# Performance work log

Hardware: AMD Instinct MI355X
Metric: run time of the kernel (lower is better)

The kernel has to match this reference:

```python
import jax, jax.numpy as jnp
import numpy as np

# Grid spacing (CartesianGrid3D.dx / .dy)
DX = 1000.0
DY = 1000.0
WENO_EPS = 1e-6  # classic Jiang-Shu smoothness regularizer

NZ, NY, NX = 32, 1024, 1024


def _weno5_recon(qm2, qm1, q0, qp1, qp2):
    """Classic WENO5 (Jiang-Shu) reconstruction of q at the i+1/2 face,
    left-biased (stencil centered on cell i)."""
    c1312 = 13.0 / 12.0
    b0 = c1312 * (qm2 - 2.0 * qm1 + q0) ** 2 + 0.25 * (qm2 - 4.0 * qm1 + 3.0 * q0) ** 2
    b1 = c1312 * (qm1 - 2.0 * q0 + qp1) ** 2 + 0.25 * (qm1 - qp1) ** 2
    b2 = c1312 * (q0 - 2.0 * qp1 + qp2) ** 2 + 0.25 * (3.0 * q0 - 4.0 * qp1 + qp2) ** 2
    a0 = 0.1 / (WENO_EPS + b0) ** 2
    a1 = 0.6 / (WENO_EPS + b1) ** 2
    a2 = 0.3 / (WENO_EPS + b2) ** 2
    p0 = (2.0 * qm2 - 7.0 * qm1 + 11.0 * q0) / 6.0
    p1 = (-qm1 + 5.0 * q0 + 2.0 * qp1) / 6.0
    p2 = (2.0 * q0 + 5.0 * qp1 - qp2) / 6.0
    return (a0 * p0 + a1 * p1 + a2 * p2) / (a0 + a1 + a2)


def _weno5_flux(q, vel, axis):
    """Upwinded WENO5 flux vel * q_face at face i+1/2 along `axis`.
    Edge-padded so the flux array has the same shape as q (faithful to
    recon.weno5_x / weno5_y producing full-shape flux arrays whose interior
    is consumed by the divergence)."""
    q = jnp.moveaxis(q, axis, -1)
    vel = jnp.moveaxis(vel, axis, -1)
    n = q.shape[-1]
    pad = [(0, 0)] * (q.ndim - 1) + [(2, 3)]
    qp = jnp.pad(q, pad, mode='edge')
    sl = lambda o: qp[..., o:o + n]
    qm2, qm1, q0, qp1, qp2, qp3 = sl(0), sl(1), sl(2), sl(3), sl(4), sl(5)
    q_left = _weno5_recon(qm2, qm1, q0, qp1, qp2)          # upwind for vel >= 0
    q_right = _weno5_recon(qp3, qp2, qp1, q0, qm1)         # mirrored, vel < 0
    f = vel * jnp.where(vel >= 0.0, q_left, q_right)
    return jnp.moveaxis(f, -1, axis)


def setup_inputs() -> dict:
    key = jax.random.key(0)
    kh, ku, kv = jax.random.split(key, 3)
    h = jax.random.normal(kh, (NZ, NY, NX), dtype=jnp.float32)
    u = jax.random.normal(ku, (NZ, NY, NX), dtype=jnp.float32)
    v = jax.random.normal(kv, (NZ, NY, NX), dtype=jnp.float32)
    return {"h": h, "u": u, "v": v}


def reference(h, u, v):
    # fe: flux through east face (x), fn: flux through north face (y)
    fe = _weno5_flux(h, u, axis=2)
    fn = _weno5_flux(h, v, axis=1)
    div = ((fe[1:-1, 2:-2, 2:-2] - fe[1:-1, 2:-2, 1:-3]) / DX
           + (fn[1:-1, 2:-2, 2:-2] - fn[1:-1, 1:-3, 2:-2]) / DY)
    out = jnp.zeros_like(h)
    out = out.at[1:-1, 2:-2, 2:-2].set(-div)
    return out
```

## Files before the change

### kernel.cpp

```cpp
#include <hip/hip_runtime.h>

#define NZ 32
#define NY 1024
#define NX 1024
#define TY 16

__device__ __forceinline__ float rcpf(float x) { return __builtin_amdgcn_rcpf(x); }

__device__ __forceinline__ float weno5(float qm2, float qm1, float q0, float qp1, float qp2) {
    const float c1312 = 13.0f / 12.0f;
    float t0 = qm2 - 2.0f * qm1 + q0;
    float u0 = qm2 - 4.0f * qm1 + 3.0f * q0;
    float b0 = c1312 * t0 * t0 + 0.25f * u0 * u0;
    float t1 = qm1 - 2.0f * q0 + qp1;
    float u1 = qm1 - qp1;
    float b1 = c1312 * t1 * t1 + 0.25f * u1 * u1;
    float t2 = q0 - 2.0f * qp1 + qp2;
    float u2 = 3.0f * q0 - 4.0f * qp1 + qp2;
    float b2 = c1312 * t2 * t2 + 0.25f * u2 * u2;
    float e0 = 1e-6f + b0;
    float e1 = 1e-6f + b1;
    float e2 = 1e-6f + b2;
    float s0 = e0 * e0, s1 = e1 * e1, s2 = e2 * e2;
    float a0 = 0.1f * (s1 * s2);
    float a1 = 0.6f * (s0 * s2);
    float a2 = 0.3f * (s0 * s1);
    const float c16 = 1.0f / 6.0f;
    float p0 = (2.0f * qm2 - 7.0f * qm1 + 11.0f * q0) * c16;
    float p1 = (-qm1 + 5.0f * q0 + 2.0f * qp1) * c16;
    float p2 = (2.0f * q0 + 5.0f * qp1 - qp2) * c16;
    return (a0 * p0 + a1 * p1 + a2 * p2) * rcpf(a0 + a1 + a2);
}

__device__ __forceinline__ float upwind_flux(float vel, float qm2, float qm1, float q0,
                                             float qp1, float qp2, float qp3) {
    bool up = vel >= 0.0f;
    float s0 = up ? qm2 : qp3;
    float s1 = up ? qm1 : qp2;
    float s2 = up ? q0  : qp1;
    float s3 = up ? qp1 : q0;
    float s4 = up ? qp2 : qm1;
    return vel * weno5(s0, s1, s2, s3, s4);
}

__global__ __launch_bounds__(256) void adv_kernel(const float* __restrict__ h,
                                                  const float* __restrict__ u,
                                                  const float* __restrict__ v,
                                                  float* __restrict__ out) {
    const int tid = threadIdx.x;
    const int x  = blockIdx.x * 256 + tid;
    const int z  = blockIdx.z;
    const int y0 = blockIdx.y * TY;
    const size_t zoff = (size_t)z * (NY * NX);
    const float* __restrict__ hz = h + zoff;
    const float* __restrict__ uz = u + zoff;
    const float* __restrict__ vz = v + zoff;
    float* __restrict__ oz = out + zoff;

    if (z == 0 || z == NZ - 1) {
#pragma unroll
        for (int t = 0; t < TY; ++t) oz[(y0 + t) * NX + x] = 0.0f;
        return;
    }

    int xc[7];
#pragma unroll
    for (int k = 0; k < 7; ++k) {
        int xx = x - 3 + k;
        xc[k] = xx < 0 ? 0 : (xx > NX - 1 ? NX - 1 : xx);
    }
    const int xm1 = (x > 0) ? x - 1 : 0;
    const bool xin = (x >= 2) && (x <= NX - 3);
    const bool lane0 = (tid & 63) == 0;

    float hy[7];
#pragma unroll
    for (int k = 0; k < 7; ++k) {
        int yy = y0 - 3 + k;
        yy = yy < 0 ? 0 : (yy > NY - 1 ? NY - 1 : yy);
        hy[k] = hz[yy * NX + x];
    }

    {
    }
    const int ym1 = (y0 > 0) ? y0 - 1 : 0;
    float fn_lo = upwind_flux(vz[ym1 * NX + x], hy[0], hy[1], hy[2], hy[3], hy[4], hy[5]);

#pragma unroll
    for (int t = 0; t < TY; ++t) {
        const int y = y0 + t;
        const int row = y * NX;

        float hx0 = hz[row + xc[0]];
        float hx1 = hz[row + xc[1]];
        float hx2 = hz[row + xc[2]];
        float hx3 = hy[3];
        float hx4 = hz[row + xc[4]];
        float hx5 = hz[row + xc[5]];
        float hx6 = hz[row + xc[6]];

        float fe_hi = upwind_flux(uz[row + x], hx1, hx2, hx3, hx4, hx5, hx6);
        float fe_lo = __shfl_up(fe_hi, 1);
        if (lane0) {
            fe_lo = upwind_flux(uz[row + xm1], hx0, hx1, hx2, hx3, hx4, hx5);
        }

        float fn_hi = upwind_flux(vz[row + x], hy[1], hy[2], hy[3], hy[4], hy[5], hy[6]);

        const float inv_d = 1.0f / 1000.0f;
        float val = -((fe_hi - fe_lo) + (fn_hi - fn_lo)) * inv_d;
        bool interior = xin && (y >= 2) && (y <= NY - 3);
        oz[row + x] = interior ? val : 0.0f;

        fn_lo = fn_hi;
#pragma unroll
        for (int k = 0; k < 6; ++k) hy[k] = hy[k + 1];
        int yn = y + 4;
        yn = yn > NY - 1 ? NY - 1 : yn;
        hy[6] = hz[yn * NX + x];
    }
}

extern "C" void kernel_launch(void* const* d_in, const int* in_sizes, int n_in,
                              void* d_out, int out_size, void* d_ws, size_t ws_size,
                              hipStream_t stream) {
    const float* h = (const float*)d_in[0];
    const float* u = (const float*)d_in[1];
    const float* v = (const float*)d_in[2];
    float* out = (float*)d_out;

    dim3 block(256, 1, 1);
    dim3 grid(NX / 256, NY / TY, NZ);
    adv_kernel<<<grid, block, 0, stream>>>(h, u, v, out);
}
```

Baseline: 440.5 us.

## Process two x-points per thread with float2 loads and halve row tile

Each thread now handles two adjacent x columns and uses float2 vectorized loads for h, u, v and the output. The x-stencil is shared between the pair, so each row needs fewer loads and the even point's lo flux comes from the odd flux computed in the same thread. TY drops from 16 to 8 to keep the number of blocks up now that each block covers 512 columns, and the WENO polynomial coefficients are pre-folded into constants. The cost is higher register pressure from two float2 y-windows and the duplicated flux computations, plus a separate boundary path that uses scalar clamped loads.

```diff
diff --git a/kernel.cpp b/kernel.cpp
--- a/kernel.cpp
+++ b/kernel.cpp
@@ -3,7 +3,7 @@
 #define NZ 32
 #define NY 1024
 #define NX 1024
-#define TY 16
+#define TY 8
 
 __device__ __forceinline__ float rcpf(float x) { return __builtin_amdgcn_rcpf(x); }
 
@@ -18,17 +18,14 @@
     float t2 = q0 - 2.0f * qp1 + qp2;
     float u2 = 3.0f * q0 - 4.0f * qp1 + qp2;
     float b2 = c1312 * t2 * t2 + 0.25f * u2 * u2;
-    float e0 = 1e-6f + b0;
-    float e1 = 1e-6f + b1;
-    float e2 = 1e-6f + b2;
+    float e0 = 1e-6f + b0, e1 = 1e-6f + b1, e2 = 1e-6f + b2;
     float s0 = e0 * e0, s1 = e1 * e1, s2 = e2 * e2;
     float a0 = 0.1f * (s1 * s2);
     float a1 = 0.6f * (s0 * s2);
     float a2 = 0.3f * (s0 * s1);
-    const float c16 = 1.0f / 6.0f;
-    float p0 = (2.0f * qm2 - 7.0f * qm1 + 11.0f * q0) * c16;
-    float p1 = (-qm1 + 5.0f * q0 + 2.0f * qp1) * c16;
-    float p2 = (2.0f * q0 + 5.0f * qp1 - qp2) * c16;
+    float p0 = (1.0f / 3.0f) * qm2 + (-7.0f / 6.0f) * qm1 + (11.0f / 6.0f) * q0;
+    float p1 = (-1.0f / 6.0f) * qm1 + (5.0f / 6.0f) * q0 + (1.0f / 3.0f) * qp1;
+    float p2 = (1.0f / 3.0f) * q0 + (5.0f / 6.0f) * qp1 + (-1.0f / 6.0f) * qp2;
     return (a0 * p0 + a1 * p1 + a2 * p2) * rcpf(a0 + a1 + a2);
 }
 
@@ -48,9 +45,10 @@
                                                   const float* __restrict__ v,
                                                   float* __restrict__ out) {
     const int tid = threadIdx.x;
-    const int x  = blockIdx.x * 256 + tid;
-    const int z  = blockIdx.z;
-    const int y0 = blockIdx.y * TY;
+    const int px  = blockIdx.x * 256 + tid;
+    const int x0  = px * 2;
+    const int z   = blockIdx.z;
+    const int y0  = blockIdx.y * TY;
     const size_t zoff = (size_t)z * (NY * NX);
     const float* __restrict__ hz = h + zoff;
     const float* __restrict__ uz = u + zoff;
@@ -59,65 +57,88 @@
 
     if (z == 0 || z == NZ - 1) {
 #pragma unroll
-        for (int t = 0; t < TY; ++t) oz[(y0 + t) * NX + x] = 0.0f;
+        for (int t = 0; t < TY; ++t)
+            *(float2*)(oz + (y0 + t) * NX + x0) = make_float2(0.0f, 0.0f);
         return;
     }
 
-    int xc[7];
-#pragma unroll
-    for (int k = 0; k < 7; ++k) {
-        int xx = x - 3 + k;
-        xc[k] = xx < 0 ? 0 : (xx > NX - 1 ? NX - 1 : xx);
-    }
-    const int xm1 = (x > 0) ? x - 1 : 0;
-    const bool xin = (x >= 2) && (x <= NX - 3);
+    const bool xfast = (x0 >= 4) && (x0 <= NX - 6);
+    const bool xint  = (px >= 1) && (px <= (NX - 4) / 2);
     const bool lane0 = (tid & 63) == 0;
 
-    float hy[7];
+    float2 hy[7];
 #pragma unroll
     for (int k = 0; k < 7; ++k) {
         int yy = y0 - 3 + k;
         yy = yy < 0 ? 0 : (yy > NY - 1 ? NY - 1 : yy);
-        hy[k] = hz[yy * NX + x];
+        hy[k] = *(const float2*)(hz + yy * NX + x0);
     }
 
-    {
-    }
     const int ym1 = (y0 > 0) ? y0 - 1 : 0;
-    float fn_lo = upwind_flux(vz[ym1 * NX + x], hy[0], hy[1], hy[2], hy[3], hy[4], hy[5]);
+    float2 vm = *(const float2*)(vz + ym1 * NX + x0);
+    float fn_lo_e = upwind_flux(vm.x, hy[0].x, hy[1].x, hy[2].x, hy[3].x, hy[4].x, hy[5].x);
+    float fn_lo_o = upwind_flux(vm.y, hy[0].y, hy[1].y, hy[2].y, hy[3].y, hy[4].y, hy[5].y);
 
 #pragma unroll
     for (int t = 0; t < TY; ++t) {
-        const int y = y0 + t;
+        const int y   = y0 + t;
         const int row = y * NX;
+        const float* __restrict__ rp  = hz + row;
+        const float* __restrict__ rpu = uz + row;
 
-        float hx0 = hz[row + xc[0]];
-        float hx1 = hz[row + xc[1]];
-        float hx2 = hz[row + xc[2]];
-        float hx3 = hy[3];
-        float hx4 = hz[row + xc[4]];
-        float hx5 = hz[row + xc[5]];
-        float hx6 = hz[row + xc[6]];
+        float sl[10];
+        if (xfast) {
+            float2 m2  = *(const float2*)(rp + x0 - 4);
+            float2 m1  = *(const float2*)(rp + x0 - 2);
+            float2 pp1 = *(const float2*)(rp + x0 + 2);
+            float2 pp2 = *(const float2*)(rp + x0 + 4);
+            sl[0] = m2.x;  sl[1] = m2.y;
+            sl[2] = m1.x;  sl[3] = m1.y;
+            sl[6] = pp1.x; sl[7] = pp1.y;
+            sl[8] = pp2.x; sl[9] = pp2.y;
+        } else {
+#pragma unroll
+            for (int k = 0; k < 10; ++k) {
+                if (k == 4 || k == 5) continue;
+                int xx = x0 - 4 + k;
+                xx = xx < 0 ? 0 : (xx > NX - 1 ? NX - 1 : xx);
+                sl[k] = rp[xx];
+            }
+        }
+        sl[4] = hy[3].x;
+        sl[5] = hy[3].y;
 
-        float fe_hi = upwind_flux(uz[row + x], hx1, hx2, hx3, hx4, hx5, hx6);
-        float fe_lo = __shfl_up(fe_hi, 1);
+        float2 uv = *(const float2*)(rpu + x0);
+        float2 vv = *(const float2*)(vz + row + x0);
+
+        float f_e = upwind_flux(uv.x, sl[2], sl[3], sl[4], sl[5], sl[6], sl[7]);
+        float f_o = upwind_flux(uv.y, sl[3], sl[4], sl[5], sl[6], sl[7], sl[8]);
+
+        float fe_lo = __shfl_up(f_o, 1);
         if (lane0) {
-            fe_lo = upwind_flux(uz[row + xm1], hx0, hx1, hx2, hx3, hx4, hx5);
+            int xm = x0 - 1;
+            xm = xm < 0 ? 0 : xm;
+            fe_lo = upwind_flux(rpu[xm], sl[1], sl[2], sl[3], sl[4], sl[5], sl[6]);
         }
 
-        float fn_hi = upwind_flux(vz[row + x], hy[1], hy[2], hy[3], hy[4], hy[5], hy[6]);
+        float fn_e = upwind_flux(vv.x, hy[1].x, hy[2].x, hy[3].x, hy[4].x, hy[5].x, hy[6].x);
+        float fn_o = upwind_flux(vv.y, hy[1].y, hy[2].y, hy[3].y, hy[4].y, hy[5].y, hy[6].y);
 
         const float inv_d = 1.0f / 1000.0f;
-        float val = -((fe_hi - fe_lo) + (fn_hi - fn_lo)) * inv_d;
-        bool interior = xin && (y >= 2) && (y <= NY - 3);
-        oz[row + x] = interior ? val : 0.0f;
+        bool yin = (y >= 2) && (y <= NY - 3);
+        bool wr  = xint && yin;
+        float2 res;
+        res.x = wr ? -((f_e - fe_lo) + (fn_e - fn_lo_e)) * inv_d : 0.0f;
+        res.y = wr ? -((f_o - f_e) + (fn_o - fn_lo_o)) * inv_d : 0.0f;
+        *(float2*)(oz + row + x0) = res;
 
-        fn_lo = fn_hi;
+        fn_lo_e = fn_e;
+        fn_lo_o = fn_o;
 #pragma unroll
         for (int k = 0; k < 6; ++k) hy[k] = hy[k + 1];
         int yn = y + 4;
         yn = yn > NY - 1 ? NY - 1 : yn;
-        hy[6] = hz[yn * NX + x];
+        hy[6] = *(const float2*)(hz + yn * NX + x0);
     }
 }
 
@@ -130,6 +151,6 @@
     float* out = (float*)d_out;
 
     dim3 block(256, 1, 1);
-    dim3 grid(NX / 256, NY / TY, NZ);
+    dim3 grid(NX / 512, NY / TY, NZ);
     adv_kernel<<<grid, block, 0, stream>>>(h, u, v, out);
 }
```

Result: faster. 396.6 us (-10.0%).
